# Kernel tuning notes

Measured on AMD Instinct MI355X. Metric: run time of the kernel, lower is better.

Reference implementation:

```python
import jax, jax.numpy as jnp
import numpy as np

VOL = (32, 64, 64)          # 3D brain volume grid
B, N, D = 2, 4096, 1024     # batch, active voxels (seq_len), feature_dim
H, KNN = 16, 16             # num_heads, num_neighbors


def setup_inputs() -> dict:
    key = jax.random.key(0)
    k1, k2, k3, k4 = jax.random.split(key, 4)
    # boolean 3D mask with exactly N active voxels (so seq_len == #active)
    rng = np.random.default_rng(0)
    flat = np.zeros(int(np.prod(VOL)), dtype=bool)
    flat[rng.choice(flat.size, N, replace=False)] = True
    visual_cortex_mask = jnp.asarray(flat.reshape(VOL))
    x = jax.random.normal(k1, (B, N, D), dtype=jnp.float32)
    s = 1.0 / np.sqrt(D)
    Wq = jax.random.normal(k2, (D, D), dtype=jnp.float32) * s
    Wk = jax.random.normal(k3, (D, D), dtype=jnp.float32) * s
    Wv = jax.random.normal(k4, (D, D), dtype=jnp.float32) * s
    return {"x": x, "visual_cortex_mask": visual_cortex_mask,
            "Wq": Wq, "Wk": Wk, "Wv": Wv}


def reference(x, visual_cortex_mask, Wq, Wk, Wv):
    batch, seq_len, d = x.shape
    hd = d // H
    # --- kNN over active voxel coordinates (cdist + topk) ---
    flat = visual_cortex_mask.reshape(-1)
    (act,) = jnp.nonzero(flat, size=seq_len)  # flat indices of active voxels
    coords = jnp.stack(jnp.unravel_index(act, visual_cortex_mask.shape),
                       axis=1).astype(jnp.float32)           # [N, 3]
    sq = jnp.sum(coords * coords, axis=-1)                    # [N]
    d2 = sq[:, None] + sq[None, :] - 2.0 * (coords @ coords.T)  # squared dists
    _, nbr = jax.lax.top_k(-d2, KNN + 1)   # smallest distances first
    nbr = nbr[:, 1:]                       # drop self -> [N, KNN] positions
    # --- QKV projections (torch Linear: x @ W.T) ---
    q = (x @ Wq.T).reshape(batch, seq_len, H, hd)
    k = (x @ Wk.T).reshape(batch, seq_len, H, hd)
    v = (x @ Wv.T).reshape(batch, seq_len, H, hd)
    # --- gather-based sparse attention: each query attends only to its
    # KNN neighbors (exactly the block-mask semantics of the original) ---
    kn = k[:, nbr]   # [B, N, KNN, H, hd]
    vn = v[:, nbr]   # [B, N, KNN, H, hd]
    scale = 1.0 / np.sqrt(hd)
    scores = jnp.einsum('bnhd,bnkhd->bhnk', q, kn) * scale
    attn = jax.nn.softmax(scores, axis=-1)
    out = jnp.einsum('bhnk,bnkhd->bnhd', attn, vn).reshape(batch, seq_len, d)
    metric = k.mean(axis=2)  # key.mean over heads -> [B, N, hd]
    return out, metric
```

## Files before the change

kernel.cpp:

```cpp
#include <hip/hip_runtime.h>
#include <hip/hip_bf16.h>
#include <stdint.h>

#define BATCH 2
#define NPTS 4096
#define DMODEL 1024
#define NHEAD 16
#define HDIM 64
#define KNN 16
#define MASKN 131072
#define EBLK 128

typedef __attribute__((ext_vector_type(8))) short bf16x8;
typedef __attribute__((ext_vector_type(4))) float f32x4;

__device__ __forceinline__ float b2f(unsigned short u) {
    union { unsigned int i; float f; } c; c.i = ((unsigned int)u) << 16; return c.f;
}
__device__ __forceinline__ unsigned short f2b(float f) {
    unsigned int x = __float_as_uint(f);
    unsigned int r = (x + 0x7fffu + ((x >> 16) & 1u)) >> 16;
    return (unsigned short)r;
}
__device__ __forceinline__ unsigned int pack2f(float a, float b) {
    return (unsigned int)f2b(a) | ((unsigned int)f2b(b) << 16);
}
__device__ __forceinline__ void gload16(const unsigned short* g, unsigned short* l) {
    __builtin_amdgcn_global_load_lds((const __attribute__((address_space(1))) void*)g,
                                     (__attribute__((address_space(3))) void*)l, 16, 0, 0);
}

__global__ __launch_bounds__(256) void count8_kernel(const unsigned char* __restrict__ m8,
                                                     int* __restrict__ cnt8) {
    __shared__ int red[256];
    const int b = blockIdx.x, t = threadIdx.x;
    const uchar4 v = ((const uchar4*)m8)[b * 256 + t];
    red[t] = (v.x != 0) + (v.y != 0) + (v.z != 0) + (v.w != 0);
    __syncthreads();
    for (int off = 128; off >= 1; off >>= 1) {
        if (t < off) red[t] += red[t + off];
        __syncthreads();
    }
    if (t == 0) cnt8[b] = red[0];
}

__global__ __launch_bounds__(256) void count32_kernel(const unsigned char* __restrict__ m8,
                                                      const int* __restrict__ cnt8,
                                                      int* __restrict__ cnt32) {
    __shared__ int red[256];
    const int b = blockIdx.x, t = threadIdx.x;
    red[t] = (t < EBLK) ? cnt8[t] : 0;
    __syncthreads();
    for (int off = 128; off >= 1; off >>= 1) {
        if (t < off) red[t] += red[t + off];
        __syncthreads();
    }
    if (red[0] == NPTS) return;
    __syncthreads();
    const int4 v = ((const int4*)m8)[b * 256 + t];
    red[t] = (v.x != 0) + (v.y != 0) + (v.z != 0) + (v.w != 0);
    __syncthreads();
    for (int off = 128; off >= 1; off >>= 1) {
        if (t < off) red[t] += red[t + off];
        __syncthreads();
    }
    if (t == 0) cnt32[b] = red[0];
}

__global__ __launch_bounds__(256) void extract_kernel(const unsigned char* __restrict__ m8,
                                                      const int* __restrict__ cnt8,
                                                      const int* __restrict__ cnt32,
                                                      int* __restrict__ act) {
    __shared__ int sblk[EBLK];
    __shared__ int sthr[256];
    const int b = blockIdx.x, t = threadIdx.x;
    if (t < EBLK) sblk[t] = cnt8[t];
    __syncthreads();
    for (int off = 1; off < EBLK; off <<= 1) {
        int v = (t < EBLK && t >= off) ? sblk[t - off] : 0;
        __syncthreads();
        if (t < EBLK) sblk[t] += v;
        __syncthreads();
    }
    const bool bytes = (sblk[EBLK - 1] == NPTS);
    if (!bytes) {
        __syncthreads();
        if (t < EBLK) sblk[t] = cnt32[t];
        __syncthreads();
        for (int off = 1; off < EBLK; off <<= 1) {
            int v = (t < EBLK && t >= off) ? sblk[t - off] : 0;
            __syncthreads();
            if (t < EBLK) sblk[t] += v;
            __syncthreads();
        }
    }
    const int blkoff = (b == 0) ? 0 : sblk[b - 1];
    const int gbase = b * 1024 + t * 4;
    int f0, f1, f2, f3;
    if (bytes) {
        const uchar4 v = ((const uchar4*)m8)[b * 256 + t];
        f0 = v.x != 0; f1 = v.y != 0; f2 = v.z != 0; f3 = v.w != 0;
    } else {
        const int4 v = ((const int4*)m8)[b * 256 + t];
        f0 = v.x != 0; f1 = v.y != 0; f2 = v.z != 0; f3 = v.w != 0;
    }
    const int c = f0 + f1 + f2 + f3;
    sthr[t] = c;
    __syncthreads();
    for (int off = 1; off < 256; off <<= 1) {
        int v = (t >= off) ? sthr[t - off] : 0;
        __syncthreads();
        sthr[t] += v;
        __syncthreads();
    }
    int pos = blkoff + sthr[t] - c;
    if (f0) act[pos++] = gbase;
    if (f1) act[pos++] = gbase + 1;
    if (f2) act[pos++] = gbase + 2;
    if (f3) act[pos++] = gbase + 3;
}

__global__ __launch_bounds__(256) void knn_kernel(const int* __restrict__ act,
                                                  int* __restrict__ nbr) {
    __shared__ int act_s[NPTS];
    const int t = threadIdx.x;
    for (int i = t; i < NPTS; i += 256) act_s[i] = act[i];
    __syncthreads();
    const int q = blockIdx.x * 16 + (t >> 4);
    const int sub = t & 15;
    const int aq = act_s[q];
    const int qz = aq >> 12, qy = (aq >> 6) & 63, qx = aq & 63;
    int best[17];
    #pragma unroll
    for (int i = 0; i < 17; ++i) best[i] = 0x7FFFFFFF;
    for (int j = sub; j < NPTS; j += 16) {
        const int aj = act_s[j];
        const int dz = (aj >> 12) - qz;
        const int dy = ((aj >> 6) & 63) - qy;
        const int dx = (aj & 63) - qx;
        const int d2 = dz * dz + dy * dy + dx * dx;
        int p = (d2 << 12) | j;
        if (p < best[16]) {
            #pragma unroll
            for (int u = 0; u < 17; ++u) {
                const bool lt = p < best[u];
                const int tmp = best[u];
                best[u] = lt ? p : best[u];
                p = lt ? tmp : p;
            }
        }
    }
    int head = best[0];
    int keep = 0;
    #pragma unroll
    for (int r = 0; r < KNN + 1; ++r) {
        int m = head;
        #pragma unroll
        for (int off = 8; off >= 1; off >>= 1) m = min(m, __shfl_xor(m, off, 16));
        if (sub == r - 1) keep = m;
        const bool win = (head == m);
        #pragma unroll
        for (int u = 0; u < 16; ++u) if (win) best[u] = best[u + 1];
        if (win) best[16] = 0x7FFFFFFF;
        head = best[0];
    }
    nbr[q * KNN + sub] = keep & 4095;
}

__global__ __launch_bounds__(256) void cast_kernel(const float* __restrict__ src,
                                                   unsigned short* __restrict__ dst, int n8) {
    const int i = blockIdx.x * 256 + threadIdx.x;
    if (i >= n8) return;
    const float4 a = ((const float4*)src)[2 * i];
    const float4 b = ((const float4*)src)[2 * i + 1];
    uint4 w;
    w.x = pack2f(a.x, a.y); w.y = pack2f(a.z, a.w);
    w.z = pack2f(b.x, b.y); w.w = pack2f(b.z, b.w);
    ((uint4*)dst)[i] = w;
}

__global__ __launch_bounds__(256) void gemm_qkv_bf16(
    const unsigned short* __restrict__ Xb,
    const unsigned short* __restrict__ Wb,
    unsigned short* __restrict__ O0, unsigned short* __restrict__ O1, unsigned short* __restrict__ O2)
{
    const int K = DMODEL, N = DMODEL;
    const unsigned short* W = Wb + (size_t)blockIdx.z * DMODEL * DMODEL;
    unsigned short* C = (blockIdx.z == 0) ? O0 : (blockIdx.z == 1) ? O1 : O2;
    __shared__ unsigned short As[2][128 * 32];
    __shared__ unsigned short Bs[2][128 * 32];
    const int tid = threadIdx.x;
    const int rowBase = blockIdx.x * 128;
    const int colBase = blockIdx.y * 128;
    const int lane = tid & 63, w = tid >> 6;
    const int wr = w >> 1, wc = w & 1;
    const int lr = lane & 15, kg = lane >> 4;

    f32x4 acc[4][4];
    const f32x4 zero = {0.f, 0.f, 0.f, 0.f};
    #pragma unroll
    for (int i = 0; i < 4; ++i)
        #pragma unroll
        for (int j = 0; j < 4; ++j) acc[i][j] = zero;

    const int srow4 = tid >> 2;
    const int xch = (tid & 3) ^ (srow4 & 3);
    const unsigned short* agp = &Xb[(size_t)(rowBase + srow4) * K + xch * 8];
    const unsigned short* bgp = &W[(size_t)(colBase + srow4) * K + xch * 8];
    unsigned short* a0[2] = { &As[0][w * 512], &As[1][w * 512] };
    unsigned short* a1[2] = { &As[0][2048 + w * 512], &As[1][2048 + w * 512] };
    unsigned short* b0[2] = { &Bs[0][w * 512], &Bs[1][w * 512] };
    unsigned short* b1[2] = { &Bs[0][2048 + w * 512], &Bs[1][2048 + w * 512] };

    #define STAGE(kt, bf) do { \
        gload16(agp + (kt) * 32,           a0[bf]); \
        gload16(agp + 64 * K + (kt) * 32,  a1[bf]); \
        gload16(bgp + (kt) * 32,           b0[bf]); \
        gload16(bgp + 64 * K + (kt) * 32,  b1[bf]); \
    } while (0)

    const int rchunk = (kg ^ (lr & 3)) * 8;

    #define COMPUTE(bf) do { \
        bf16x8 af[4], bfr[4]; \
        _Pragma("unroll") \
        for (int mi = 0; mi < 4; ++mi) \
            af[mi] = *(const bf16x8*)&As[bf][(wr * 64 + mi * 16 + lr) * 32 + rchunk]; \
        _Pragma("unroll") \
        for (int ni = 0; ni < 4; ++ni) \
            bfr[ni] = *(const bf16x8*)&Bs[bf][(wc * 64 + ni * 16 + lr) * 32 + rchunk]; \
        __builtin_amdgcn_s_setprio(1); \
        _Pragma("unroll") \
        for (int mi = 0; mi < 4; ++mi) \
            _Pragma("unroll") \
            for (int ni = 0; ni < 4; ++ni) \
                acc[mi][ni] = __builtin_amdgcn_mfma_f32_16x16x32_bf16(af[mi], bfr[ni], acc[mi][ni], 0, 0, 0); \
        __builtin_amdgcn_s_setprio(0); \
    } while (0)

    STAGE(0, 0);
    STAGE(1, 1);
    for (int kt = 0; kt < 30; ++kt) {
        const int bf = kt & 1;
        asm volatile("s_waitcnt vmcnt(4)" ::: "memory");
        __builtin_amdgcn_s_barrier();
        COMPUTE(bf);
        __builtin_amdgcn_s_barrier();
        STAGE(kt + 2, bf);
    }
    asm volatile("s_waitcnt vmcnt(4)" ::: "memory");
    __builtin_amdgcn_s_barrier();
    COMPUTE(0);
    __builtin_amdgcn_s_barrier();
    asm volatile("s_waitcnt vmcnt(0)" ::: "memory");
    __builtin_amdgcn_s_barrier();
    COMPUTE(1);
    #undef STAGE
    #undef COMPUTE

    #pragma unroll
    for (int mi = 0; mi < 4; ++mi)
        #pragma unroll
        for (int ni = 0; ni < 4; ++ni) {
            const int row0 = rowBase + wr * 64 + mi * 16 + kg * 4;
            const int col = colBase + wc * 64 + ni * 16 + lr;
            #pragma unroll
            for (int j = 0; j < 4; ++j)
                C[(size_t)(row0 + j) * N + col] = f2b(acc[mi][ni][j]);
        }
}

__device__ __forceinline__ void stage16(unsigned short* dst, const float* src) {
    const float4 a = ((const float4*)src)[0];
    const float4 b = ((const float4*)src)[1];
    const float4 c = ((const float4*)src)[2];
    const float4 d = ((const float4*)src)[3];
    uint4 w0, w1;
    w0.x = pack2f(a.x, a.y); w0.y = pack2f(a.z, a.w);
    w0.z = pack2f(b.x, b.y); w0.w = pack2f(b.z, b.w);
    w1.x = pack2f(c.x, c.y); w1.y = pack2f(c.z, c.w);
    w1.z = pack2f(d.x, d.y); w1.w = pack2f(d.z, d.w);
    ((uint4*)dst)[0] = w0;
    ((uint4*)dst)[1] = w1;
}

__global__ __launch_bounds__(256) void gemm_qkv_f32(
    const float* __restrict__ X,
    const float* __restrict__ W0, const float* __restrict__ W1, const float* __restrict__ W2,
    unsigned short* __restrict__ O0, unsigned short* __restrict__ O1, unsigned short* __restrict__ O2)
{
    const int K = DMODEL, N = DMODEL;
    const float* W = (blockIdx.z == 0) ? W0 : (blockIdx.z == 1) ? W1 : W2;
    unsigned short* C = (blockIdx.z == 0) ? O0 : (blockIdx.z == 1) ? O1 : O2;
    __shared__ unsigned short As[128 * 32];
    __shared__ unsigned short Bs[128 * 32];
    const int tid = threadIdx.x;
    const int rowBase = blockIdx.x * 128;
    const int colBase = blockIdx.y * 128;
    const int lane = tid & 63, w = tid >> 6;
    const int wr = w >> 1, wc = w & 1;
    const int lr = lane & 15, kg = lane >> 4;
    const int srow = tid >> 1;
    const int scol = (tid & 1) * 16;
    f32x4 acc[4][4];
    const f32x4 zero = {0.f, 0.f, 0.f, 0.f};
    #pragma unroll
    for (int i = 0; i < 4; ++i)
        #pragma unroll
        for (int j = 0; j < 4; ++j) acc[i][j] = zero;
    const float* Arow = &X[(size_t)(rowBase + srow) * K + scol];
    const float* Brow = &W[(size_t)(colBase + srow) * K + scol];
    unsigned short* Adst = &As[srow * 32 + scol];
    unsigned short* Bdst = &Bs[srow * 32 + scol];
    for (int kb = 0; kb < K; kb += 32) {
        __syncthreads();
        stage16(Adst, Arow + kb);
        stage16(Bdst, Brow + kb);
        __syncthreads();
        bf16x8 af[4], bfr[4];
        #pragma unroll
        for (int mi = 0; mi < 4; ++mi)
            af[mi] = *(const bf16x8*)&As[(wr * 64 + mi * 16 + lr) * 32 + kg * 8];
        #pragma unroll
        for (int ni = 0; ni < 4; ++ni)
            bfr[ni] = *(const bf16x8*)&Bs[(wc * 64 + ni * 16 + lr) * 32 + kg * 8];
        #pragma unroll
        for (int mi = 0; mi < 4; ++mi)
            #pragma unroll
            for (int ni = 0; ni < 4; ++ni)
                acc[mi][ni] = __builtin_amdgcn_mfma_f32_16x16x32_bf16(af[mi], bfr[ni], acc[mi][ni], 0, 0, 0);
    }
    #pragma unroll
    for (int mi = 0; mi < 4; ++mi)
        #pragma unroll
        for (int ni = 0; ni < 4; ++ni) {
            const int row0 = rowBase + wr * 64 + mi * 16 + kg * 4;
            const int col = colBase + wc * 64 + ni * 16 + lr;
            #pragma unroll
            for (int j = 0; j < 4; ++j)
                C[(size_t)(row0 + j) * N + col] = f2b(acc[mi][ni][j]);
        }
}

__global__ __launch_bounds__(256) void attn_kernel(
    const unsigned short* __restrict__ Q, const unsigned short* __restrict__ Kb,
    const unsigned short* __restrict__ Vb, const int* __restrict__ nbr,
    float* __restrict__ out)
{
    const int n = blockIdx.x;
    const int b = blockIdx.y;
    __shared__ unsigned short k_s[128][KNN][8];
    __shared__ unsigned short q_s[DMODEL];
    __shared__ float a_s[NHEAD][KNN];
    __shared__ int nb_s[KNN];
    const int tid = threadIdx.x;
    if (tid < KNN) nb_s[tid] = nbr[n * KNN + tid];
    *(int2*)&q_s[tid * 4] = *(const int2*)&Q[((size_t)b * NPTS + n) * DMODEL + tid * 4];
    __syncthreads();
    {
        const int kk = tid & 15;
        const int c0 = tid >> 4;
        const unsigned short* krow = &Kb[((size_t)b * NPTS + nb_s[kk]) * DMODEL];
        #pragma unroll
        for (int i = 0; i < 8; ++i) {
            const int c = c0 + 16 * i;
            *(uint4*)&k_s[c][kk][0] = *(const uint4*)&krow[c * 8];
        }
    }
    const int o = tid * 4;
    ushort4 vpre[KNN];
    #pragma unroll
    for (int k2 = 0; k2 < KNN; ++k2)
        vpre[k2] = *(const ushort4*)&Vb[((size_t)b * NPTS + nb_s[k2]) * DMODEL + o];
    __syncthreads();
    const int h = tid >> 4, kk = tid & 15;
    float s = 0.f;
    #pragma unroll
    for (int j = 0; j < 8; ++j) {
        const bf16x8 qq = *(const bf16x8*)&q_s[h * HDIM + j * 8];
        const bf16x8 kr = *(const bf16x8*)&k_s[h * 8 + j][kk][0];
        #pragma unroll
        for (int e = 0; e < 8; ++e)
            s += b2f((unsigned short)qq[e]) * b2f((unsigned short)kr[e]);
    }
    s *= 0.125f;
    float m = s;
    #pragma unroll
    for (int off = 8; off >= 1; off >>= 1) m = fmaxf(m, __shfl_xor(m, off, 16));
    const float e = __expf(s - m);
    float sum = e;
    #pragma unroll
    for (int off = 8; off >= 1; off >>= 1) sum += __shfl_xor(sum, off, 16);
    a_s[h][kk] = e / sum;
    __syncthreads();
    const int h2 = tid >> 4;
    float av0 = 0.f, av1 = 0.f, av2 = 0.f, av3 = 0.f;
    #pragma unroll
    for (int k2 = 0; k2 < KNN; ++k2) {
        const float a = a_s[h2][k2];
        av0 += a * b2f(vpre[k2].x); av1 += a * b2f(vpre[k2].y);
        av2 += a * b2f(vpre[k2].z); av3 += a * b2f(vpre[k2].w);
    }
    float4 r; r.x = av0; r.y = av1; r.z = av2; r.w = av3;
    *(float4*)&out[((size_t)b * NPTS + n) * DMODEL + o] = r;
}

__global__ __launch_bounds__(256) void metric_kernel(const unsigned short* __restrict__ Kb,
                                                     float* __restrict__ mout) {
    const int i = blockIdx.x * 256 + threadIdx.x;
    if (i >= BATCH * NPTS * HDIM) return;
    const int d = i & 63;
    const int bn = i >> 6;
    const unsigned short* kp = &Kb[(size_t)bn * DMODEL + d];
    float s = 0.f;
    #pragma unroll
    for (int hh = 0; hh < NHEAD; ++hh) s += b2f(kp[hh * HDIM]);
    mout[i] = s * 0.0625f;
}

extern "C" void kernel_launch(void* const* d_in, const int* in_sizes, int n_in,
                              void* d_out, int out_size, void* d_ws, size_t ws_size,
                              hipStream_t stream) {
    const float* x = (const float*)d_in[0];
    const unsigned char* mask = (const unsigned char*)d_in[1];
    const float* Wq = (const float*)d_in[2];
    const float* Wk = (const float*)d_in[3];
    const float* Wv = (const float*)d_in[4];
    float* out = (float*)d_out;
    char* ws = (char*)d_ws;

    const size_t QKV_BYTES = (size_t)BATCH * NPTS * DMODEL * 2;
    const size_t XB_BYTES  = (size_t)BATCH * NPTS * DMODEL * 2;
    const size_t WB_BYTES  = (size_t)3 * DMODEL * DMODEL * 2;
    unsigned short* qb = (unsigned short*)(ws);
    unsigned short* kb = (unsigned short*)(ws + QKV_BYTES);
    unsigned short* vb = (unsigned short*)(ws + 2 * QKV_BYTES);
    const size_t SMALL_BYTES = (size_t)NPTS * sizeof(int) * (1 + KNN) + 2 * EBLK * sizeof(int);
    const size_t need_base = 3 * QKV_BYTES + SMALL_BYTES;
    const size_t need_full = need_base + XB_BYTES + WB_BYTES;
    const bool full = (ws_size >= need_full);
    char* tail = ws + 3 * QKV_BYTES;
    unsigned short* Xb = (unsigned short*)tail;
    unsigned short* Wb = (unsigned short*)(tail + XB_BYTES);
    char* small = full ? (tail + XB_BYTES + WB_BYTES) : tail;
    int* act  = (int*)small;
    int* nbr  = (int*)(small + NPTS * sizeof(int));
    int* cnt8 = (int*)(small + NPTS * sizeof(int) * (1 + KNN));
    int* cnt32 = cnt8 + EBLK;
    if (ws_size < need_base) return;

    count8_kernel<<<EBLK, 256, 0, stream>>>(mask, cnt8);
    count32_kernel<<<EBLK, 256, 0, stream>>>(mask, cnt8, cnt32);
    extract_kernel<<<EBLK, 256, 0, stream>>>(mask, cnt8, cnt32, act);
    knn_kernel<<<256, 256, 0, stream>>>(act, nbr);
    if (full) {
        const int xn8 = BATCH * NPTS * DMODEL / 8;
        const int wn8 = DMODEL * DMODEL / 8;
        cast_kernel<<<(xn8 + 255) / 256, 256, 0, stream>>>(x, Xb, xn8);
        cast_kernel<<<(wn8 + 255) / 256, 256, 0, stream>>>(Wq, Wb, wn8);
        cast_kernel<<<(wn8 + 255) / 256, 256, 0, stream>>>(Wk, Wb + (size_t)DMODEL * DMODEL, wn8);
        cast_kernel<<<(wn8 + 255) / 256, 256, 0, stream>>>(Wv, Wb + (size_t)2 * DMODEL * DMODEL, wn8);
        gemm_qkv_bf16<<<dim3(64, 8, 3), 256, 0, stream>>>(Xb, Wb, qb, kb, vb);
    } else {
        gemm_qkv_f32<<<dim3(64, 8, 3), 256, 0, stream>>>(x, Wq, Wk, Wv, qb, kb, vb);
    }
    attn_kernel<<<dim3(NPTS, BATCH), 256, 0, stream>>>(qb, kb, vb, nbr, out);
    metric_kernel<<<(BATCH * NPTS * HDIM + 255) / 256, 256, 0, stream>>>(kb, out + (size_t)BATCH * NPTS * DMODEL);
}
```

Measured before the change: 202.4 us.

## Fuse cast launches and enlarge QKV GEMM tile with triple-buffered loads

Merges the four fp32-to-bf16 cast launches into one kernel that indexes x and the three weight matrices. Reworks the bf16 QKV GEMM to 512-thread blocks covering 256x128 tiles, with a three-stage LDS ring buffer and adjusted vmcnt waits. The aim is fewer launches, more reuse of each staged W tile, and deeper prefetch to hide global latency. In exchange LDS use per block rises and the grid halves to 768 blocks, which may reduce occupancy.

```diff
diff --git a/kernel.cpp b/kernel.cpp
--- a/kernel.cpp
+++ b/kernel.cpp
@@ -167,19 +167,36 @@
     nbr[q * KNN + sub] = keep & 4095;
 }
 
-__global__ __launch_bounds__(256) void cast_kernel(const float* __restrict__ src,
-                                                   unsigned short* __restrict__ dst, int n8) {
+#define XN8 (BATCH * NPTS * DMODEL / 8)
+#define WN8 (DMODEL * DMODEL / 8)
+__global__ __launch_bounds__(256) void cast_all_kernel(
+    const float* __restrict__ x, const float* __restrict__ wq,
+    const float* __restrict__ wk, const float* __restrict__ wv,
+    unsigned short* __restrict__ Xb, unsigned short* __restrict__ Wb) {
     const int i = blockIdx.x * 256 + threadIdx.x;
-    if (i >= n8) return;
-    const float4 a = ((const float4*)src)[2 * i];
-    const float4 b = ((const float4*)src)[2 * i + 1];
+    const int total = XN8 + 3 * WN8;
+    if (i >= total) return;
+    const float* src;
+    unsigned short* dst;
+    if (i < XN8) {
+        src = x + (size_t)i * 8;
+        dst = Xb + (size_t)i * 8;
+    } else {
+        const int j = i - XN8;
+        const int wsel = j >> 17;
+        const int o = j & (WN8 - 1);
+        src = ((wsel == 0) ? wq : (wsel == 1) ? wk : wv) + (size_t)o * 8;
+        dst = Wb + ((size_t)wsel * WN8 + o) * 8;
+    }
+    const float4 a = ((const float4*)src)[0];
+    const float4 b = ((const float4*)src)[1];
     uint4 w;
     w.x = pack2f(a.x, a.y); w.y = pack2f(a.z, a.w);
     w.z = pack2f(b.x, b.y); w.w = pack2f(b.z, b.w);
-    ((uint4*)dst)[i] = w;
-}
-
-__global__ __launch_bounds__(256) void gemm_qkv_bf16(
+    *(uint4*)dst = w;
+}
+
+__global__ __launch_bounds__(512, 4) void gemm_qkv_bf16(
     const unsigned short* __restrict__ Xb,
     const unsigned short* __restrict__ Wb,
     unsigned short* __restrict__ O0, unsigned short* __restrict__ O1, unsigned short* __restrict__ O2)
@@ -187,10 +204,10 @@
     const int K = DMODEL, N = DMODEL;
     const unsigned short* W = Wb + (size_t)blockIdx.z * DMODEL * DMODEL;
     unsigned short* C = (blockIdx.z == 0) ? O0 : (blockIdx.z == 1) ? O1 : O2;
-    __shared__ unsigned short As[2][128 * 32];
-    __shared__ unsigned short Bs[2][128 * 32];
+    __shared__ unsigned short As[3][256 * 32];
+    __shared__ unsigned short Bs[3][128 * 32];
     const int tid = threadIdx.x;
-    const int rowBase = blockIdx.x * 128;
+    const int rowBase = blockIdx.x * 256;
     const int colBase = blockIdx.y * 128;
     const int lane = tid & 63, w = tid >> 6;
     const int wr = w >> 1, wc = w & 1;
@@ -207,16 +224,11 @@
     const int xch = (tid & 3) ^ (srow4 & 3);
     const unsigned short* agp = &Xb[(size_t)(rowBase + srow4) * K + xch * 8];
     const unsigned short* bgp = &W[(size_t)(colBase + srow4) * K + xch * 8];
-    unsigned short* a0[2] = { &As[0][w * 512], &As[1][w * 512] };
-    unsigned short* a1[2] = { &As[0][2048 + w * 512], &As[1][2048 + w * 512] };
-    unsigned short* b0[2] = { &Bs[0][w * 512], &Bs[1][w * 512] };
-    unsigned short* b1[2] = { &Bs[0][2048 + w * 512], &Bs[1][2048 + w * 512] };
 
     #define STAGE(kt, bf) do { \
-        gload16(agp + (kt) * 32,           a0[bf]); \
-        gload16(agp + 64 * K + (kt) * 32,  a1[bf]); \
-        gload16(bgp + (kt) * 32,           b0[bf]); \
-        gload16(bgp + 64 * K + (kt) * 32,  b1[bf]); \
+        gload16(agp + (kt) * 32,            &As[bf][w * 512]); \
+        gload16(agp + 128 * K + (kt) * 32,  &As[bf][4096 + w * 512]); \
+        gload16(bgp + (kt) * 32,            &Bs[bf][w * 512]); \
     } while (0)
 
     const int rchunk = (kg ^ (lr & 3)) * 8;
@@ -238,25 +250,36 @@
         __builtin_amdgcn_s_setprio(0); \
     } while (0)
 
+    #define ITER(kt, bf) do { \
+        asm volatile("s_waitcnt vmcnt(6)" ::: "memory"); \
+        __builtin_amdgcn_s_barrier(); \
+        COMPUTE(bf); \
+        __builtin_amdgcn_s_barrier(); \
+        STAGE((kt) + 3, bf); \
+    } while (0)
+
     STAGE(0, 0);
     STAGE(1, 1);
-    for (int kt = 0; kt < 30; ++kt) {
-        const int bf = kt & 1;
-        asm volatile("s_waitcnt vmcnt(4)" ::: "memory");
-        __builtin_amdgcn_s_barrier();
-        COMPUTE(bf);
-        __builtin_amdgcn_s_barrier();
-        STAGE(kt + 2, bf);
-    }
-    asm volatile("s_waitcnt vmcnt(4)" ::: "memory");
+    STAGE(2, 2);
+    for (int kt3 = 0; kt3 < 27; kt3 += 3) {
+        ITER(kt3 + 0, 0);
+        ITER(kt3 + 1, 1);
+        ITER(kt3 + 2, 2);
+    }
+    ITER(27, 0);
+    ITER(28, 1);
+    asm volatile("s_waitcnt vmcnt(6)" ::: "memory");
+    __builtin_amdgcn_s_barrier();
+    COMPUTE(2);
+    asm volatile("s_waitcnt vmcnt(3)" ::: "memory");
     __builtin_amdgcn_s_barrier();
     COMPUTE(0);
-    __builtin_amdgcn_s_barrier();
     asm volatile("s_waitcnt vmcnt(0)" ::: "memory");
     __builtin_amdgcn_s_barrier();
     COMPUTE(1);
     #undef STAGE
     #undef COMPUTE
+    #undef ITER
 
     #pragma unroll
     for (int mi = 0; mi < 4; ++mi)
@@ -454,13 +477,9 @@
     extract_kernel<<<EBLK, 256, 0, stream>>>(mask, cnt8, cnt32, act);
     knn_kernel<<<256, 256, 0, stream>>>(act, nbr);
     if (full) {
-        const int xn8 = BATCH * NPTS * DMODEL / 8;
-        const int wn8 = DMODEL * DMODEL / 8;
-        cast_kernel<<<(xn8 + 255) / 256, 256, 0, stream>>>(x, Xb, xn8);
-        cast_kernel<<<(wn8 + 255) / 256, 256, 0, stream>>>(Wq, Wb, wn8);
-        cast_kernel<<<(wn8 + 255) / 256, 256, 0, stream>>>(Wk, Wb + (size_t)DMODEL * DMODEL, wn8);
-        cast_kernel<<<(wn8 + 255) / 256, 256, 0, stream>>>(Wv, Wb + (size_t)2 * DMODEL * DMODEL, wn8);
-        gemm_qkv_bf16<<<dim3(64, 8, 3), 256, 0, stream>>>(Xb, Wb, qb, kb, vb);
+        const int castN = XN8 + 3 * WN8;
+        cast_all_kernel<<<(castN + 255) / 256, 256, 0, stream>>>(x, Wq, Wk, Wv, Xb, Wb);
+        gemm_qkv_bf16<<<dim3(32, 8, 3), 512, 0, stream>>>(Xb, Wb, qb, kb, vb);
     } else {
         gemm_qkv_f32<<<dim3(64, 8, 3), 256, 0, stream>>>(x, Wq, Wk, Wv, qb, kb, vb);
     }
```

Result: faster. 197.1 us (-2.6%).
